# Kernel tuning notes

Hardware: AMD Instinct MI355X
Metric: run time of the kernel (lower is better)

## Reference

```python
import jax, jax.numpy as jnp
import numpy as np


def gcn_conv(x, src, dst, W, b, num_nodes):
    # PyG GCNConv with add_self_loops=True, symmetric normalization.
    # src/dst already include self-loops.
    ones = jnp.ones(src.shape[0], dtype=x.dtype)
    deg = jax.ops.segment_sum(ones, dst, num_segments=num_nodes)  # [N]
    dinv = jnp.where(deg > 0, jax.lax.rsqrt(deg), 0.0)
    norm = dinv[src] * dinv[dst]                                   # [E+N]
    h = x @ W                                                      # [N, out]
    msg = h[src] * norm[:, None]                                   # gather + scale
    out = jax.ops.segment_sum(msg, dst, num_segments=num_nodes)    # scatter-add
    return out + b


def setup_inputs() -> dict:
    key = jax.random.key(0)
    k1, k2, k3, k4 = jax.random.split(key, 4)
    N, E = 50000, 1600000
    IN, HID, OUT = 1536, 256, 128
    x = jax.random.normal(k1, (N, IN), dtype=jnp.float32)
    edge_index = jax.random.randint(k2, (2, E), 0, N, dtype=jnp.int64)
    # Glorot-style scaled weights
    W1 = jax.random.normal(k3, (IN, HID), dtype=jnp.float32) / np.sqrt(IN)
    W2 = jax.random.normal(k4, (HID, OUT), dtype=jnp.float32) / np.sqrt(HID)
    b1 = jnp.zeros((HID,), dtype=jnp.float32)
    b2 = jnp.zeros((OUT,), dtype=jnp.float32)
    return {"x": x, "edge_index": edge_index, "W1": W1, "b1": b1,
            "W2": W2, "b2": b2, "num_nodes": N}


def reference(x, edge_index, W1, b1, W2, b2, num_nodes):
    loop = jnp.arange(num_nodes, dtype=edge_index.dtype)
    src = jnp.concatenate([edge_index[0], loop])
    dst = jnp.concatenate([edge_index[1], loop])
    h = gcn_conv(x, src, dst, W1, b1, num_nodes)
    h = jax.nn.relu(h)
    h = gcn_conv(h, src, dst, W2, b2, num_nodes)
    # F.normalize(h, dim=1): x / max(||x||_2, 1e-12)
    nrm = jnp.linalg.norm(h, axis=1, keepdims=True)
    return h / jnp.maximum(nrm, 1e-12)
```

## Files before the change

kernel.cpp:

```cpp
#include <hip/hip_runtime.h>

typedef __attribute__((ext_vector_type(4))) float f32x4;
typedef __attribute__((ext_vector_type(2))) float f32x2;
typedef __attribute__((ext_vector_type(8))) short s16x8;
typedef __attribute__((ext_vector_type(4))) unsigned short u16x4;

static __device__ __forceinline__ unsigned short f2bf(float f) {
  unsigned int u = __builtin_bit_cast(unsigned int, f);
  u += 0x7fffu + ((u >> 16) & 1u);
  return (unsigned short)(u >> 16);
}
static __device__ __forceinline__ float bf2f(unsigned short h) {
  unsigned int u = ((unsigned int)h) << 16;
  return __builtin_bit_cast(float, u);
}

static __device__ __forceinline__ void gload_lds16(const void* g, void* l) {
  __builtin_amdgcn_global_load_lds(
      (const __attribute__((address_space(1))) unsigned int*)g,
      (__attribute__((address_space(3))) unsigned int*)l, 16, 0, 0);
}

__global__ void zero_k(int* p, int n) {
  int i = blockIdx.x * 256 + threadIdx.x;
  if (i < n) p[i] = 0;
}
__global__ void deg_count_k(const int* __restrict__ edges, int* cnt, int E) {
  int e = blockIdx.x * 256 + threadIdx.x;
  if (e < E) atomicAdd(&cnt[edges[E + e]], 1);
}
__global__ void dinv_k(const int* __restrict__ cnt, float* dinv, int N) {
  int i = blockIdx.x * 256 + threadIdx.x;
  if (i < N) dinv[i] = rsqrtf((float)(cnt[i] + 1));
}

__global__ __launch_bounds__(256) void scan1_k(const int* __restrict__ cnt,
                                               int* __restrict__ loc,
                                               int* __restrict__ bsum, int N) {
  int t = threadIdx.x;
  int i0 = blockIdx.x * 1024 + t * 4;
  int c[4];
#pragma unroll
  for (int j = 0; j < 4; ++j) c[j] = (i0 + j < N) ? cnt[i0 + j] : 0;
  int tsum = c[0] + c[1] + c[2] + c[3];
  int lane = t & 63, wv = t >> 6;
  int incl = tsum;
#pragma unroll
  for (int off = 1; off < 64; off <<= 1) {
    int u = __shfl_up(incl, off, 64);
    if (lane >= off) incl += u;
  }
  __shared__ int ws[4];
  if (lane == 63) ws[wv] = incl;
  __syncthreads();
  int wbase = 0;
  for (int w = 0; w < wv; ++w) wbase += ws[w];
  int run = wbase + incl - tsum;
#pragma unroll
  for (int j = 0; j < 4; ++j) {
    if (i0 + j < N) loc[i0 + j] = run;
    run += c[j];
  }
  if (t == 255) bsum[blockIdx.x] = wbase + incl;
}
__global__ void scan2_k(int* bsum, int nb) {
  int lane = threadIdx.x;
  int v = (lane < nb) ? bsum[lane] : 0;
  int incl = v;
#pragma unroll
  for (int off = 1; off < 64; off <<= 1) {
    int u = __shfl_up(incl, off, 64);
    if (lane >= off) incl += u;
  }
  if (lane < nb) bsum[lane] = incl - v;
}
__global__ void addoff_k(int* loc, int* cursor, const int* __restrict__ bsum, int N) {
  int i = blockIdx.x * 256 + threadIdx.x;
  if (i < N) {
    int v = loc[i] + bsum[i >> 10];
    loc[i] = v;
    cursor[i] = v;
  }
}
__global__ void fill_k(const int* __restrict__ edges, int* cursor,
                       int* __restrict__ csr, int E) {
  int e = blockIdx.x * 256 + threadIdx.x;
  if (e < E) {
    int s = edges[e], d = edges[E + e];
    int pos = atomicAdd(&cursor[d], 1);
    csr[pos] = s;
  }
}

__global__ void convw_k(const float* __restrict__ W, unsigned short* __restrict__ Wt, int K, int Nn) {
  int t = blockIdx.x * 256 + threadIdx.x;
  if (t < K * Nn) {
    int n = t / K;
    int k = t - n * K;
    Wt[n * K + k] = f2bf(W[(long long)k * Nn + n]);
  }
}

template <int KTOT, int NTOT, bool A_BF16>
__global__ __launch_bounds__(256, 2) void gemm_k(
    const void* __restrict__ Aptr, const unsigned short* __restrict__ Bt,
    const float* __restrict__ dinv, unsigned short* __restrict__ outg, int M) {
  constexpr int BM = 128, BK = 32;
  constexpr int LDA = BK + 8;
  constexpr int STRIP = NTOT / 4;
  constexpr int NF = STRIP / 16;
  constexpr int BCH = (NTOT / 16) / 4;
  constexpr int ACH = (BM / 16) / 4;
  constexpr int NT = KTOT / BK;

  __shared__ unsigned short Asm_[2][BM * LDA];
  __shared__ unsigned short Bsm_[2][NTOT * BK];

  const int tid = threadIdx.x;
  const int wave = tid >> 6;
  const int lane = tid & 63;
  const int fr = lane & 15;
  const int quad = lane >> 4;
  const int m0 = blockIdx.x * BM;

  f32x4 acc[8][NF];
#pragma unroll
  for (int i = 0; i < 8; ++i)
#pragma unroll
    for (int j = 0; j < NF; ++j) { f32x4 z = {0.f, 0.f, 0.f, 0.f}; acc[i][j] = z; }

  const int sl_r = lane >> 2;
  const int sl_s = (lane & 3) ^ ((lane >> 3) & 3);

  auto stageB = [&](int k0, int buf) {
#pragma unroll
    for (int c = 0; c < BCH; ++c) {
      int cc = wave * BCH + c;
      int r = cc * 16 + sl_r;
      const unsigned short* gp = Bt + (long long)r * KTOT + k0 + sl_s * 8;
      gload_lds16(gp, &Bsm_[buf][cc * 512]);
    }
  };
  auto stageA_h = [&](int k0, int buf) {
    const unsigned short* Ah = (const unsigned short*)Aptr;
#pragma unroll
    for (int c = 0; c < ACH; ++c) {
      int cc = wave * ACH + c;
      int r = cc * 16 + sl_r;
      const unsigned short* gp = Ah + (long long)(m0 + r) * KTOT + k0 + sl_s * 8;
      gload_lds16(gp, &Asm_[buf][cc * 512]);
    }
  };

  const int sr = tid >> 1;
  const int sc = (tid & 1) << 4;
  const bool arow_ok = (m0 + sr) < M;
  const float* arowf = (const float*)Aptr + (long long)(m0 + sr) * KTOT;
  float va[16];
  auto loadA = [&](int k0) {
    if (arow_ok) {
      const f32x4* p = (const f32x4*)(arowf + k0 + sc);
      f32x4 v0 = p[0], v1 = p[1], v2 = p[2], v3 = p[3];
#pragma unroll
      for (int j = 0; j < 4; ++j) { va[j] = v0[j]; va[4 + j] = v1[j]; va[8 + j] = v2[j]; va[12 + j] = v3[j]; }
    } else {
#pragma unroll
      for (int j = 0; j < 16; ++j) va[j] = 0.0f;
    }
  };
  auto cvtWriteA = [&](int buf) {
    s16x8 h0, h1;
#pragma unroll
    for (int j = 0; j < 8; ++j) { h0[j] = (short)f2bf(va[j]); h1[j] = (short)f2bf(va[8 + j]); }
    *(s16x8*)&Asm_[buf][sr * LDA + sc] = h0;
    *(s16x8*)&Asm_[buf][sr * LDA + sc + 8] = h1;
  };

  stageB(0, 0);
  if constexpr (A_BF16) {
    stageA_h(0, 0);
  } else {
    loadA(0);
    cvtWriteA(0);
    if (NT > 1) loadA(BK);
  }

  const int xsl = (fr >> 1) & 3;
  for (int kt = 0; kt < NT; ++kt) {
    const int cur = kt & 1;
    __syncthreads();
    if (kt + 1 < NT) {
      stageB((kt + 1) * BK, cur ^ 1);
      if constexpr (A_BF16) {
        stageA_h((kt + 1) * BK, cur ^ 1);
      } else {
        cvtWriteA(cur ^ 1);
        if (kt + 2 < NT) loadA((kt + 2) * BK);
      }
    }

    s16x8 af[8], bfr[NF];
#pragma unroll
    for (int mi = 0; mi < 8; ++mi) {
      if constexpr (A_BF16)
        af[mi] = *(const s16x8*)&Asm_[cur][(mi * 16 + fr) * BK + ((quad ^ xsl) << 3)];
      else
        af[mi] = *(const s16x8*)&Asm_[cur][(mi * 16 + fr) * LDA + quad * 8];
    }
#pragma unroll
    for (int ni = 0; ni < NF; ++ni)
      bfr[ni] = *(const s16x8*)&Bsm_[cur][(wave * STRIP + ni * 16 + fr) * BK + ((quad ^ xsl) << 3)];
#pragma unroll
    for (int mi = 0; mi < 8; ++mi)
#pragma unroll
      for (int ni = 0; ni < NF; ++ni)
        acc[mi][ni] = __builtin_amdgcn_mfma_f32_16x16x32_bf16(af[mi], bfr[ni], acc[mi][ni], 0, 0, 0);
  }

#pragma unroll
  for (int mi = 0; mi < 8; ++mi) {
    int mbase = mi * 16 + quad * 4;
#pragma unroll
    for (int r = 0; r < 4; ++r) {
      int gm = m0 + mbase + r;
      if (gm < M) {
        float dv = dinv[gm];
#pragma unroll
        for (int ni = 0; ni < NF; ++ni) {
          int col = wave * STRIP + ni * 16 + fr;
          outg[(long long)gm * NTOT + col] = f2bf(acc[mi][ni][r] * dv);
        }
      }
    }
  }
}

__global__ __launch_bounds__(256) void agg1_k(const int* __restrict__ csr,
                                              const int* __restrict__ row,
                                              const int* __restrict__ cnt,
                                              const unsigned short* __restrict__ g,
                                              const float* __restrict__ bias,
                                              const float* __restrict__ dinv,
                                              unsigned short* __restrict__ h, int N) {
  const int wave = threadIdx.x >> 6, lane = threadIdx.x & 63;
  const int grp = lane >> 5, sub = lane & 31;
  const int node = blockIdx.x * 8 + wave * 2 + grp;
  if (node >= N) return;
  const int f0 = sub * 8;
  s16x8 sv = *(const s16x8*)&g[(long long)node * 256 + f0];
  float s[8];
#pragma unroll
  for (int k = 0; k < 8; ++k) s[k] = bf2f((unsigned short)sv[k]);
  const int start = row[node], len = cnt[node];
  int j = 0;
  for (; j + 8 <= len; j += 8) {
    int idx[8];
#pragma unroll
    for (int t = 0; t < 8; ++t) idx[t] = csr[start + j + t];
    s16x8 v[8];
#pragma unroll
    for (int t = 0; t < 8; ++t) v[t] = *(const s16x8*)&g[(long long)idx[t] * 256 + f0];
#pragma unroll
    for (int t = 0; t < 8; ++t)
#pragma unroll
      for (int k = 0; k < 8; ++k) s[k] += bf2f((unsigned short)v[t][k]);
  }
  for (; j < len; ++j) {
    int i0 = csr[start + j];
    s16x8 v = *(const s16x8*)&g[(long long)i0 * 256 + f0];
#pragma unroll
    for (int k = 0; k < 8; ++k) s[k] += bf2f((unsigned short)v[k]);
  }
  const float dv = dinv[node];
  f32x4 b0 = *(const f32x4*)&bias[f0];
  f32x4 b1v = *(const f32x4*)&bias[f0 + 4];
  s16x8 o;
#pragma unroll
  for (int k = 0; k < 4; ++k) o[k] = (short)f2bf(fmaxf(0.0f, b0[k] + dv * s[k]));
#pragma unroll
  for (int k = 0; k < 4; ++k) o[4 + k] = (short)f2bf(fmaxf(0.0f, b1v[k] + dv * s[4 + k]));
  *(s16x8*)&h[(long long)node * 256 + f0] = o;
}

__global__ __launch_bounds__(256) void agg2_k(const int* __restrict__ csr,
                                              const int* __restrict__ row,
                                              const int* __restrict__ cnt,
                                              const unsigned short* __restrict__ g,
                                              const float* __restrict__ b2,
                                              const float* __restrict__ dinv,
                                              float* __restrict__ out, int N) {
  const int wave = threadIdx.x >> 6, lane = threadIdx.x & 63;
  const int grp = lane >> 4, sub = lane & 15;
  const int node = blockIdx.x * 16 + wave * 4 + grp;
  if (node >= N) return;
  const int f0 = sub * 8;
  s16x8 sv = *(const s16x8*)&g[(long long)node * 128 + f0];
  float s[8];
#pragma unroll
  for (int k = 0; k < 8; ++k) s[k] = bf2f((unsigned short)sv[k]);
  const int start = row[node], len = cnt[node];
  int j = 0;
  for (; j + 8 <= len; j += 8) {
    int idx[8];
#pragma unroll
    for (int t = 0; t < 8; ++t) idx[t] = csr[start + j + t];
    s16x8 v[8];
#pragma unroll
    for (int t = 0; t < 8; ++t) v[t] = *(const s16x8*)&g[(long long)idx[t] * 128 + f0];
#pragma unroll
    for (int t = 0; t < 8; ++t)
#pragma unroll
      for (int k = 0; k < 8; ++k) s[k] += bf2f((unsigned short)v[t][k]);
  }
  for (; j < len; ++j) {
    int i0 = csr[start + j];
    s16x8 v = *(const s16x8*)&g[(long long)i0 * 128 + f0];
#pragma unroll
    for (int k = 0; k < 8; ++k) s[k] += bf2f((unsigned short)v[k]);
  }
  const float dv = dinv[node];
  f32x4 b0 = *(const f32x4*)&b2[f0];
  f32x4 b1v = *(const f32x4*)&b2[f0 + 4];
  float x[8];
#pragma unroll
  for (int k = 0; k < 4; ++k) x[k] = b0[k] + dv * s[k];
#pragma unroll
  for (int k = 0; k < 4; ++k) x[4 + k] = b1v[k] + dv * s[4 + k];
  float ss = 0.0f;
#pragma unroll
  for (int k = 0; k < 8; ++k) ss += x[k] * x[k];
#pragma unroll
  for (int off = 1; off < 16; off <<= 1) ss += __shfl_xor(ss, off, 64);
  const float inv = 1.0f / fmaxf(sqrtf(ss), 1e-12f);
  f32x4 o0 = {x[0] * inv, x[1] * inv, x[2] * inv, x[3] * inv};
  f32x4 o1 = {x[4] * inv, x[5] * inv, x[6] * inv, x[7] * inv};
  *(f32x4*)&out[(long long)node * 128 + f0] = o0;
  *(f32x4*)&out[(long long)node * 128 + f0 + 4] = o1;
}

extern "C" void kernel_launch(void* const* d_in, const int* in_sizes, int n_in,
                              void* d_out, int out_size, void* d_ws, size_t ws_size,
                              hipStream_t stream) {
  const float* x = (const float*)d_in[0];
  const int* edges = (const int*)d_in[1];
  const float* W1 = (const float*)d_in[2];
  const float* b1 = (const float*)d_in[3];
  const float* W2 = (const float*)d_in[4];
  const float* b2 = (const float*)d_in[5];
  float* out = (float*)d_out;

  const int HID = in_sizes[3];
  const int OUT = in_sizes[5];
  const int IN = in_sizes[2] / HID;
  const int N = in_sizes[0] / IN;
  const int E = in_sizes[1] / 2;

  size_t off = 0;
  auto carve = [&](size_t bytes) {
    void* p = (char*)d_ws + off;
    off += (bytes + 255) & ~(size_t)255;
    return p;
  };
  int* cnt = (int*)carve((size_t)N * 4);
  int* cursor = (int*)carve((size_t)N * 4);
  int* row = (int*)carve((size_t)N * 4);
  int* bsum = (int*)carve(64 * 4);
  int* csr = (int*)carve((size_t)E * 4 + 1024);
  float* dinv = (float*)carve((size_t)N * 4);
  unsigned short* W1t = (unsigned short*)carve((size_t)IN * HID * 2);
  unsigned short* W2t = (unsigned short*)carve((size_t)HID * OUT * 2);
  unsigned short* g1 = (unsigned short*)carve((size_t)N * HID * 2);
  unsigned short* acc1 = (unsigned short*)carve((size_t)N * HID * 2);
  unsigned short* g2 = (unsigned short*)carve((size_t)N * OUT * 2);
  (void)ws_size; (void)n_in; (void)out_size;

  const int nb = (N + 1023) / 1024;

  zero_k<<<(N + 255) / 256, 256, 0, stream>>>(cnt, N);
  deg_count_k<<<(E + 255) / 256, 256, 0, stream>>>(edges, cnt, E);
  dinv_k<<<(N + 255) / 256, 256, 0, stream>>>(cnt, dinv, N);

  scan1_k<<<nb, 256, 0, stream>>>(cnt, row, bsum, N);
  scan2_k<<<1, 64, 0, stream>>>(bsum, nb);
  addoff_k<<<(N + 255) / 256, 256, 0, stream>>>(row, cursor, bsum, N);
  fill_k<<<(E + 255) / 256, 256, 0, stream>>>(edges, cursor, csr, E);

  convw_k<<<(IN * HID + 255) / 256, 256, 0, stream>>>(W1, W1t, IN, HID);
  convw_k<<<(HID * OUT + 255) / 256, 256, 0, stream>>>(W2, W2t, HID, OUT);

  int mtiles = (N + 127) / 128;
  gemm_k<1536, 256, false><<<mtiles, 256, 0, stream>>>(x, W1t, dinv, g1, N);
  agg1_k<<<(N + 7) / 8, 256, 0, stream>>>(csr, row, cnt, g1, b1, dinv, acc1, N);
  gemm_k<256, 128, true><<<mtiles, 256, 0, stream>>>(acc1, W2t, dinv, g2, N);
  agg2_k<<<(N + 15) / 16, 256, 0, stream>>>(csr, row, cnt, g2, b2, dinv, out, N);
}
```

Before: 845.0 us.

## Shrink GEMM tile, split neighbor lists across wave lanes, tile weight transpose

The GEMM row tile drops from 128 to 64 with higher launch-bounds occupancy, which gives more blocks over 50k rows. The aggregation kernels now give one wave per node and split its edge list across lane groups, then combine the partial sums with cross-lane shuffles. This is meant to balance variable-degree work and raise memory-level parallelism. The dinv computation is fused into addoff, and the weight transpose now uses a shared-memory tiled transpose. The risks are more tail masking work, redundant lanes during the epilogue, and a smaller GEMM tile that reuses B less.

New measurement: 866.7 us. +2.6%, slower.

```diff
diff --git a/kernel.cpp b/kernel.cpp
--- a/kernel.cpp
+++ b/kernel.cpp
@@ -3,7 +3,6 @@
 typedef __attribute__((ext_vector_type(4))) float f32x4;
 typedef __attribute__((ext_vector_type(2))) float f32x2;
 typedef __attribute__((ext_vector_type(8))) short s16x8;
-typedef __attribute__((ext_vector_type(4))) unsigned short u16x4;
 
 static __device__ __forceinline__ unsigned short f2bf(float f) {
   unsigned int u = __builtin_bit_cast(unsigned int, f);
@@ -28,10 +27,6 @@
 __global__ void deg_count_k(const int* __restrict__ edges, int* cnt, int E) {
   int e = blockIdx.x * 256 + threadIdx.x;
   if (e < E) atomicAdd(&cnt[edges[E + e]], 1);
-}
-__global__ void dinv_k(const int* __restrict__ cnt, float* dinv, int N) {
-  int i = blockIdx.x * 256 + threadIdx.x;
-  if (i < N) dinv[i] = rsqrtf((float)(cnt[i] + 1));
 }
 
 __global__ __launch_bounds__(256) void scan1_k(const int* __restrict__ cnt,
@@ -74,12 +69,14 @@
   }
   if (lane < nb) bsum[lane] = incl - v;
 }
-__global__ void addoff_k(int* loc, int* cursor, const int* __restrict__ bsum, int N) {
+__global__ void addoff_k(int* loc, int* cursor, const int* __restrict__ bsum,
+                         const int* __restrict__ cnt, float* __restrict__ dinv, int N) {
   int i = blockIdx.x * 256 + threadIdx.x;
   if (i < N) {
     int v = loc[i] + bsum[i >> 10];
     loc[i] = v;
     cursor[i] = v;
+    dinv[i] = rsqrtf((float)(cnt[i] + 1));
   }
 }
 __global__ void fill_k(const int* __restrict__ edges, int* cursor,
@@ -92,26 +89,35 @@
   }
 }
 
-__global__ void convw_k(const float* __restrict__ W, unsigned short* __restrict__ Wt, int K, int Nn) {
-  int t = blockIdx.x * 256 + threadIdx.x;
-  if (t < K * Nn) {
-    int n = t / K;
-    int k = t - n * K;
-    Wt[n * K + k] = f2bf(W[(long long)k * Nn + n]);
-  }
-}
-
-template <int KTOT, int NTOT, bool A_BF16>
-__global__ __launch_bounds__(256, 2) void gemm_k(
+__global__ __launch_bounds__(256) void convw_k(const float* __restrict__ W,
+                                               unsigned short* __restrict__ Wt,
+                                               int K, int Nn) {
+  __shared__ float t[32][33];
+  const int tx = threadIdx.x & 31, ty = threadIdx.x >> 5;
+  const int k0 = blockIdx.x * 32, n0 = blockIdx.y * 32;
+#pragma unroll
+  for (int r = 0; r < 32; r += 8)
+    t[r + ty][tx] = W[(long long)(k0 + r + ty) * Nn + (n0 + tx)];
+  __syncthreads();
+#pragma unroll
+  for (int r = 0; r < 32; r += 8)
+    Wt[(long long)(n0 + r + ty) * K + (k0 + tx)] = f2bf(t[tx][r + ty]);
+}
+
+template <int KTOT, int NTOT, int BM, bool A_BF16>
+__global__ __launch_bounds__(256, 3) void gemm_k(
     const void* __restrict__ Aptr, const unsigned short* __restrict__ Bt,
     const float* __restrict__ dinv, unsigned short* __restrict__ outg, int M) {
-  constexpr int BM = 128, BK = 32;
+  constexpr int BK = 32;
   constexpr int LDA = BK + 8;
+  constexpr int MI = BM / 16;
   constexpr int STRIP = NTOT / 4;
   constexpr int NF = STRIP / 16;
   constexpr int BCH = (NTOT / 16) / 4;
   constexpr int ACH = (BM / 16) / 4;
   constexpr int NT = KTOT / BK;
+  constexpr int TPR = 256 / BM;
+  constexpr int FPT = BK / TPR;
 
   __shared__ unsigned short Asm_[2][BM * LDA];
   __shared__ unsigned short Bsm_[2][NTOT * BK];
@@ -123,9 +129,9 @@
   const int quad = lane >> 4;
   const int m0 = blockIdx.x * BM;
 
-  f32x4 acc[8][NF];
-#pragma unroll
-  for (int i = 0; i < 8; ++i)
+  f32x4 acc[MI][NF];
+#pragma unroll
+  for (int i = 0; i < MI; ++i)
 #pragma unroll
     for (int j = 0; j < NF; ++j) { f32x4 z = {0.f, 0.f, 0.f, 0.f}; acc[i][j] = z; }
 
@@ -152,28 +158,32 @@
     }
   };
 
-  const int sr = tid >> 1;
-  const int sc = (tid & 1) << 4;
+  const int sr = tid / TPR;
+  const int sc = (tid % TPR) * FPT;
   const bool arow_ok = (m0 + sr) < M;
   const float* arowf = (const float*)Aptr + (long long)(m0 + sr) * KTOT;
-  float va[16];
+  float va[FPT];
   auto loadA = [&](int k0) {
     if (arow_ok) {
-      const f32x4* p = (const f32x4*)(arowf + k0 + sc);
-      f32x4 v0 = p[0], v1 = p[1], v2 = p[2], v3 = p[3];
-#pragma unroll
-      for (int j = 0; j < 4; ++j) { va[j] = v0[j]; va[4 + j] = v1[j]; va[8 + j] = v2[j]; va[12 + j] = v3[j]; }
+#pragma unroll
+      for (int c = 0; c < FPT / 4; ++c) {
+        f32x4 v = *(const f32x4*)(arowf + k0 + sc + c * 4);
+#pragma unroll
+        for (int j = 0; j < 4; ++j) va[c * 4 + j] = v[j];
+      }
     } else {
 #pragma unroll
-      for (int j = 0; j < 16; ++j) va[j] = 0.0f;
+      for (int j = 0; j < FPT; ++j) va[j] = 0.0f;
     }
   };
   auto cvtWriteA = [&](int buf) {
-    s16x8 h0, h1;
-#pragma unroll
-    for (int j = 0; j < 8; ++j) { h0[j] = (short)f2bf(va[j]); h1[j] = (short)f2bf(va[8 + j]); }
-    *(s16x8*)&Asm_[buf][sr * LDA + sc] = h0;
-    *(s16x8*)&Asm_[buf][sr * LDA + sc + 8] = h1;
+#pragma unroll
+    for (int c = 0; c < FPT / 8; ++c) {
+      s16x8 h;
+#pragma unroll
+      for (int j = 0; j < 8; ++j) h[j] = (short)f2bf(va[c * 8 + j]);
+      *(s16x8*)&Asm_[buf][sr * LDA + sc + c * 8] = h;
+    }
   };
 
   stageB(0, 0);
@@ -199,9 +209,9 @@
       }
     }
 
-    s16x8 af[8], bfr[NF];
-#pragma unroll
-    for (int mi = 0; mi < 8; ++mi) {
+    s16x8 af[MI], bfr[NF];
+#pragma unroll
+    for (int mi = 0; mi < MI; ++mi) {
       if constexpr (A_BF16)
         af[mi] = *(const s16x8*)&Asm_[cur][(mi * 16 + fr) * BK + ((quad ^ xsl) << 3)];
       else
@@ -211,14 +221,14 @@
     for (int ni = 0; ni < NF; ++ni)
       bfr[ni] = *(const s16x8*)&Bsm_[cur][(wave * STRIP + ni * 16 + fr) * BK + ((quad ^ xsl) << 3)];
 #pragma unroll
-    for (int mi = 0; mi < 8; ++mi)
+    for (int mi = 0; mi < MI; ++mi)
 #pragma unroll
       for (int ni = 0; ni < NF; ++ni)
         acc[mi][ni] = __builtin_amdgcn_mfma_f32_16x16x32_bf16(af[mi], bfr[ni], acc[mi][ni], 0, 0, 0);
   }
 
 #pragma unroll
-  for (int mi = 0; mi < 8; ++mi) {
+  for (int mi = 0; mi < MI; ++mi) {
     int mbase = mi * 16 + quad * 4;
 #pragma unroll
     for (int r = 0; r < 4; ++r) {
@@ -243,43 +253,52 @@
                                               const float* __restrict__ dinv,
                                               unsigned short* __restrict__ h, int N) {
   const int wave = threadIdx.x >> 6, lane = threadIdx.x & 63;
+  const int node = blockIdx.x * 4 + wave;
+  if (node >= N) return;
   const int grp = lane >> 5, sub = lane & 31;
-  const int node = blockIdx.x * 8 + wave * 2 + grp;
-  if (node >= N) return;
   const int f0 = sub * 8;
-  s16x8 sv = *(const s16x8*)&g[(long long)node * 256 + f0];
   float s[8];
 #pragma unroll
-  for (int k = 0; k < 8; ++k) s[k] = bf2f((unsigned short)sv[k]);
+  for (int k = 0; k < 8; ++k) s[k] = 0.0f;
   const int start = row[node], len = cnt[node];
   int j = 0;
   for (; j + 8 <= len; j += 8) {
-    int idx[8];
-#pragma unroll
-    for (int t = 0; t < 8; ++t) idx[t] = csr[start + j + t];
-    s16x8 v[8];
-#pragma unroll
-    for (int t = 0; t < 8; ++t) v[t] = *(const s16x8*)&g[(long long)idx[t] * 256 + f0];
-#pragma unroll
-    for (int t = 0; t < 8; ++t)
+    int idx[4];
+#pragma unroll
+    for (int t = 0; t < 4; ++t) idx[t] = csr[start + j + t * 2 + grp];
+    s16x8 v[4];
+#pragma unroll
+    for (int t = 0; t < 4; ++t) v[t] = *(const s16x8*)&g[(long long)idx[t] * 256 + f0];
+#pragma unroll
+    for (int t = 0; t < 4; ++t)
 #pragma unroll
       for (int k = 0; k < 8; ++k) s[k] += bf2f((unsigned short)v[t][k]);
   }
-  for (; j < len; ++j) {
-    int i0 = csr[start + j];
-    s16x8 v = *(const s16x8*)&g[(long long)i0 * 256 + f0];
-#pragma unroll
-    for (int k = 0; k < 8; ++k) s[k] += bf2f((unsigned short)v[k]);
-  }
+  for (; j < len; j += 2) {
+    int jt = j + grp;
+    bool val = jt < len;
+    int idx = csr[start + (val ? jt : 0)];
+    s16x8 v = *(const s16x8*)&g[(long long)idx * 256 + f0];
+    float m = val ? 1.0f : 0.0f;
+#pragma unroll
+    for (int k = 0; k < 8; ++k) s[k] += m * bf2f((unsigned short)v[k]);
+  }
+#pragma unroll
+  for (int k = 0; k < 8; ++k) s[k] += __shfl_xor(s[k], 32, 64);
+  s16x8 sv = *(const s16x8*)&g[(long long)node * 256 + f0];
+#pragma unroll
+  for (int k = 0; k < 8; ++k) s[k] += bf2f((unsigned short)sv[k]);
   const float dv = dinv[node];
   f32x4 b0 = *(const f32x4*)&bias[f0];
   f32x4 b1v = *(const f32x4*)&bias[f0 + 4];
-  s16x8 o;
-#pragma unroll
-  for (int k = 0; k < 4; ++k) o[k] = (short)f2bf(fmaxf(0.0f, b0[k] + dv * s[k]));
-#pragma unroll
-  for (int k = 0; k < 4; ++k) o[4 + k] = (short)f2bf(fmaxf(0.0f, b1v[k] + dv * s[4 + k]));
-  *(s16x8*)&h[(long long)node * 256 + f0] = o;
+  if (grp == 0) {
+    s16x8 o;
+#pragma unroll
+    for (int k = 0; k < 4; ++k) o[k] = (short)f2bf(fmaxf(0.0f, b0[k] + dv * s[k]));
+#pragma unroll
+    for (int k = 0; k < 4; ++k) o[4 + k] = (short)f2bf(fmaxf(0.0f, b1v[k] + dv * s[4 + k]));
+    *(s16x8*)&h[(long long)node * 256 + f0] = o;
+  }
 }
 
 __global__ __launch_bounds__(256) void agg2_k(const int* __restrict__ csr,
@@ -290,34 +309,43 @@
                                               const float* __restrict__ dinv,
                                               float* __restrict__ out, int N) {
   const int wave = threadIdx.x >> 6, lane = threadIdx.x & 63;
+  const int node = blockIdx.x * 4 + wave;
+  if (node >= N) return;
   const int grp = lane >> 4, sub = lane & 15;
-  const int node = blockIdx.x * 16 + wave * 4 + grp;
-  if (node >= N) return;
   const int f0 = sub * 8;
-  s16x8 sv = *(const s16x8*)&g[(long long)node * 128 + f0];
   float s[8];
 #pragma unroll
-  for (int k = 0; k < 8; ++k) s[k] = bf2f((unsigned short)sv[k]);
+  for (int k = 0; k < 8; ++k) s[k] = 0.0f;
   const int start = row[node], len = cnt[node];
   int j = 0;
   for (; j + 8 <= len; j += 8) {
-    int idx[8];
-#pragma unroll
-    for (int t = 0; t < 8; ++t) idx[t] = csr[start + j + t];
-    s16x8 v[8];
-#pragma unroll
-    for (int t = 0; t < 8; ++t) v[t] = *(const s16x8*)&g[(long long)idx[t] * 128 + f0];
-#pragma unroll
-    for (int t = 0; t < 8; ++t)
+    int idx[2];
+#pragma unroll
+    for (int t = 0; t < 2; ++t) idx[t] = csr[start + j + t * 4 + grp];
+    s16x8 v[2];
+#pragma unroll
+    for (int t = 0; t < 2; ++t) v[t] = *(const s16x8*)&g[(long long)idx[t] * 128 + f0];
+#pragma unroll
+    for (int t = 0; t < 2; ++t)
 #pragma unroll
       for (int k = 0; k < 8; ++k) s[k] += bf2f((unsigned short)v[t][k]);
   }
-  for (; j < len; ++j) {
-    int i0 = csr[start + j];
-    s16x8 v = *(const s16x8*)&g[(long long)i0 * 128 + f0];
-#pragma unroll
-    for (int k = 0; k < 8; ++k) s[k] += bf2f((unsigned short)v[k]);
-  }
+  for (; j < len; j += 4) {
+    int jt = j + grp;
+    bool val = jt < len;
+    int idx = csr[start + (val ? jt : 0)];
+    s16x8 v = *(const s16x8*)&g[(long long)idx * 128 + f0];
+    float m = val ? 1.0f : 0.0f;
+#pragma unroll
+    for (int k = 0; k < 8; ++k) s[k] += m * bf2f((unsigned short)v[k]);
+  }
+#pragma unroll
+  for (int k = 0; k < 8; ++k) s[k] += __shfl_xor(s[k], 16, 64);
+#pragma unroll
+  for (int k = 0; k < 8; ++k) s[k] += __shfl_xor(s[k], 32, 64);
+  s16x8 sv = *(const s16x8*)&g[(long long)node * 128 + f0];
+#pragma unroll
+  for (int k = 0; k < 8; ++k) s[k] += bf2f((unsigned short)sv[k]);
   const float dv = dinv[node];
   f32x4 b0 = *(const f32x4*)&b2[f0];
   f32x4 b1v = *(const f32x4*)&b2[f0 + 4];
@@ -332,10 +360,12 @@
 #pragma unroll
   for (int off = 1; off < 16; off <<= 1) ss += __shfl_xor(ss, off, 64);
   const float inv = 1.0f / fmaxf(sqrtf(ss), 1e-12f);
-  f32x4 o0 = {x[0] * inv, x[1] * inv, x[2] * inv, x[3] * inv};
-  f32x4 o1 = {x[4] * inv, x[5] * inv, x[6] * inv, x[7] * inv};
-  *(f32x4*)&out[(long long)node * 128 + f0] = o0;
-  *(f32x4*)&out[(long long)node * 128 + f0 + 4] = o1;
+  if (grp == 0) {
+    f32x4 o0 = {x[0] * inv, x[1] * inv, x[2] * inv, x[3] * inv};
+    f32x4 o1 = {x[4] * inv, x[5] * inv, x[6] * inv, x[7] * inv};
+    *(f32x4*)&out[(long long)node * 128 + f0] = o0;
+    *(f32x4*)&out[(long long)node * 128 + f0 + 4] = o1;
+  }
 }
 
 extern "C" void kernel_launch(void* const* d_in, const int* in_sizes, int n_in,
@@ -378,19 +408,19 @@
 
   zero_k<<<(N + 255) / 256, 256, 0, stream>>>(cnt, N);
   deg_count_k<<<(E + 255) / 256, 256, 0, stream>>>(edges, cnt, E);
-  dinv_k<<<(N + 255) / 256, 256, 0, stream>>>(cnt, dinv, N);
 
   scan1_k<<<nb, 256, 0, stream>>>(cnt, row, bsum, N);
   scan2_k<<<1, 64, 0, stream>>>(bsum, nb);
-  addoff_k<<<(N + 255) / 256, 256, 0, stream>>>(row, cursor, bsum, N);
+  addoff_k<<<(N + 255) / 256, 256, 0, stream>>>(row, cursor, bsum, cnt, dinv, N);
   fill_k<<<(E + 255) / 256, 256, 0, stream>>>(edges, cursor, csr, E);
 
-  convw_k<<<(IN * HID + 255) / 256, 256, 0, stream>>>(W1, W1t, IN, HID);
-  convw_k<<<(HID * OUT + 255) / 256, 256, 0, stream>>>(W2, W2t, HID, OUT);
-
-  int mtiles = (N + 127) / 128;
-  gemm_k<1536, 256, false><<<mtiles, 256, 0, stream>>>(x, W1t, dinv, g1, N);
-  agg1_k<<<(N + 7) / 8, 256, 0, stream>>>(csr, row, cnt, g1, b1, dinv, acc1, N);
-  gemm_k<256, 128, true><<<mtiles, 256, 0, stream>>>(acc1, W2t, dinv, g2, N);
-  agg2_k<<<(N + 15) / 16, 256, 0, stream>>>(csr, row, cnt, g2, b2, dinv, out, N);
-}
+  convw_k<<<dim3(IN / 32, HID / 32), 256, 0, stream>>>(W1, W1t, IN, HID);
+  convw_k<<<dim3(HID / 32, OUT / 32), 256, 0, stream>>>(W2, W2t, HID, OUT);
+
+  constexpr int BM = 64;
+  int mtiles = (N + BM - 1) / BM;
+  gemm_k<1536, 256, BM, false><<<mtiles, 256, 0, stream>>>(x, W1t, dinv, g1, N);
+  agg1_k<<<(N + 3) / 4, 256, 0, stream>>>(csr, row, cnt, g1, b1, dinv, acc1, N);
+  gemm_k<256, 128, BM, true><<<mtiles, 256, 0, stream>>>(acc1, W2t, dinv, g2, N);
+  agg2_k<<<(N + 3) / 4, 256, 0, stream>>>(csr, row, cnt, g2, b2, dinv, out, N);
+}
```
